# Kernel tuning notes

Hardware: AMD Instinct MI355X
Metric: run time of the kernel (lower is better)

Reference implementation:

```python
import jax, jax.numpy as jnp
import numpy as np

D_IN = 1024
D_OUT = 1024
N_HEADS = 16
D_K = D_OUT // N_HEADS
ROPE_THETA = 10000.0


def setup_inputs() -> dict:
    key = jax.random.key(0)
    ks = jax.random.split(key, 5)
    x = jax.random.normal(ks[0], (2, 2048, D_IN), dtype=jnp.float32)
    token_positions = jnp.arange(2048, dtype=jnp.int32)
    scale = 0.02
    wq = jax.random.normal(ks[1], (D_OUT, D_IN), dtype=jnp.float32) * scale
    wk = jax.random.normal(ks[2], (D_OUT, D_IN), dtype=jnp.float32) * scale
    wv = jax.random.normal(ks[3], (D_OUT, D_IN), dtype=jnp.float32) * scale
    wo = jax.random.normal(ks[4], (D_OUT, D_OUT), dtype=jnp.float32) * scale
    return {"x": x, "token_positions": token_positions, "wq": wq, "wk": wk, "wv": wv, "wo": wo}


def _rope(x, token_positions):
    # x: [..., S, d_k]; token_positions: [S]
    d_k = x.shape[-1]
    idx = jnp.arange(d_k)
    k = idx // 2
    # thetas[i, j] = pos_i / theta^(2*(j//2)/d_k)
    angles = token_positions[:, None].astype(x.dtype) / jnp.power(
        jnp.asarray(ROPE_THETA, x.dtype), 2.0 * k.astype(x.dtype) / d_k
    )  # [S, d_k]
    cos = jnp.cos(angles)
    sin = jnp.sin(angles) * jnp.where(idx % 2 == 0, -1.0, 1.0).astype(x.dtype)
    pair_swaps = idx + jnp.where(idx % 2 == 0, 1, -1)  # swap even/odd pairs
    return x * cos + x[..., pair_swaps] * sin


def _forward(x, token_positions, wq, wk, wv, wo):
    B, S, _ = x.shape
    # fused QKV projection (same math as concat + split)
    q = jnp.einsum("bsd,od->bso", x, wq)
    k = jnp.einsum("bsd,od->bso", x, wk)
    v = jnp.einsum("bsd,od->bso", x, wv)
    # split heads: [B, S, H*dk] -> [B, H, S, dk]
    split = lambda t: t.reshape(B, S, N_HEADS, D_K).transpose(0, 2, 1, 3)
    q, k, v = split(q), split(k), split(v)
    q = _rope(q, token_positions)
    k = _rope(k, token_positions)
    scores = jnp.einsum("bhqd,bhkd->bhqk", q, k) / jnp.sqrt(jnp.asarray(D_K, x.dtype))
    causal = jnp.tril(jnp.ones((S, S), dtype=bool))
    scores = jnp.where(causal, scores, -jnp.inf)
    probs = jax.nn.softmax(scores, axis=-1)
    ctx = jnp.einsum("bhqk,bhkd->bhqd", probs, v)
    merged = ctx.transpose(0, 2, 1, 3).reshape(B, S, D_OUT)
    return jnp.einsum("bsm,om->bso", merged, wo)


def reference(x, token_positions, wq, wk, wv, wo):
    return _forward(x, token_positions, wq, wk, wv, wo)
```

## Files before the change

### kernel.cpp

```cpp
#include <hip/hip_runtime.h>

#define D_MODEL 1024
#define SEQ     2048
#define BATCH   2
#define NHEADS  16
#define DK      64
#define NROWS   (BATCH*SEQ)

typedef unsigned short u16;
typedef __bf16 bf16x8 __attribute__((ext_vector_type(8)));
typedef float  f32x4  __attribute__((ext_vector_type(4)));

__device__ __forceinline__ u16 f2bf(float f) {
    union { float f; unsigned u; } v; v.f = f;
    unsigned u = v.u;
    u += 0x7fffu + ((u >> 16) & 1);
    return (u16)(u >> 16);
}
__device__ __forceinline__ float bf2f(u16 h) {
    union { unsigned u; float f; } v; v.u = ((unsigned)h) << 16;
    return v.f;
}
__device__ __forceinline__ unsigned cvtpk_bf16(float lo, float hi) {
    unsigned r;
    asm("v_cvt_pk_bf16_f32 %0, %1, %2" : "=v"(r) : "v"(lo), "v"(hi));
    return r;
}

__device__ __forceinline__ void gload_lds16(const u16* g, u16* l) {
    __builtin_amdgcn_global_load_lds(
        (const __attribute__((address_space(1))) void*)g,
        (__attribute__((address_space(3))) void*)l, 16, 0, 0);
}

__global__ void cvt_bf16_all(const float* __restrict__ x,
                             const float* __restrict__ w0, const float* __restrict__ w1,
                             const float* __restrict__ w2, const float* __restrict__ w3,
                             u16* __restrict__ xb, u16* __restrict__ wb) {
    int i = blockIdx.x * blockDim.x + threadIdx.x;
    int row = i >> 8;
    int c   = (i & 255) * 4;
    const float* src; u16* dst;
    if (row < 4096) {
        src = x + (size_t)row * 1024;
        dst = xb + (size_t)row * 1024;
    } else {
        int r2 = row - 4096;
        int ws = r2 >> 10;
        int rr = r2 & 1023;
        const float* wsrc = ws == 0 ? w0 : ws == 1 ? w1 : ws == 2 ? w2 : w3;
        src = wsrc + (size_t)rr * 1024;
        dst = wb + ((size_t)ws << 20) + (size_t)rr * 1024;
    }
    float4 v = *(const float4*)(src + c);
    uint2 o;
    o.x = (unsigned)f2bf(v.x) | ((unsigned)f2bf(v.y) << 16);
    o.y = (unsigned)f2bf(v.z) | ((unsigned)f2bf(v.w) << 16);
    *(uint2*)(dst + c) = o;
}

__global__ __launch_bounds__(256) void gemm_qkv_p(
    const u16* __restrict__ A, const u16* __restrict__ W,
    u16* __restrict__ Qp, u16* __restrict__ Kp, u16* __restrict__ Vt)
{
    __shared__ __align__(16) u16 Ash[128 * 32];
    __shared__ __align__(16) u16 Bsh[128 * 32];

    const int m0  = blockIdx.x * 128;
    const int sel = blockIdx.y >> 3;
    const int n0  = (blockIdx.y & 7) * 128;
    const u16* B = W + ((size_t)sel << 20);
    const int tid = threadIdx.x;
    const int lane = tid & 63;
    const int w    = tid >> 6;
    const int wr = w >> 1, wc = w & 1;
    const int fr = lane & 15;
    const int fk = (lane >> 4) * 8;
    const int rsub = lane >> 2;
    const int csub = (lane & 3) * 8;

    f32x4 acc[4][4];
#pragma unroll
    for (int i = 0; i < 4; ++i)
#pragma unroll
        for (int j = 0; j < 4; ++j) acc[i][j] = (f32x4){0.f, 0.f, 0.f, 0.f};

    for (int k0 = 0; k0 < 1024; k0 += 32) {
        __syncthreads();
        const u16* Ab = A + (size_t)(m0 + 16 * w + rsub) * 1024 + k0 + csub;
        const u16* Bb = B + (size_t)(n0 + 16 * w + rsub) * 1024 + k0 + csub;
#pragma unroll
        for (int half = 0; half < 2; ++half) {
            size_t ro = (size_t)(half * 64) * 1024;
            int lo = (half * 64 + 16 * w) * 32;
            gload_lds16(Ab + ro, &Ash[lo]);
            gload_lds16(Bb + ro, &Bsh[lo]);
        }
        __syncthreads();

        bf16x8 ah[4], bh[4];
#pragma unroll
        for (int i = 0; i < 4; ++i)
            ah[i] = *(const bf16x8*)&Ash[(wr * 64 + i * 16 + fr) * 32 + fk];
#pragma unroll
        for (int j = 0; j < 4; ++j)
            bh[j] = *(const bf16x8*)&Bsh[(wc * 64 + j * 16 + fr) * 32 + fk];
#pragma unroll
        for (int i = 0; i < 4; ++i)
#pragma unroll
            for (int j = 0; j < 4; ++j)
                acc[i][j] = __builtin_amdgcn_mfma_f32_16x16x32_bf16(ah[i], bh[j], acc[i][j], 0, 0, 0);
    }

    const int r0 = (lane >> 4) * 4;
#pragma unroll
    for (int i = 0; i < 4; ++i) {
#pragma unroll
        for (int j = 0; j < 4; ++j) {
            int col = n0 + wc * 64 + j * 16 + fr;
#pragma unroll
            for (int r = 0; r < 4; ++r) {
                int row = m0 + wr * 64 + i * 16 + r0 + r;
                u16 v = f2bf(acc[i][j][r]);
                if (sel == 0)      Qp[(size_t)row * 1024 + col] = v;
                else if (sel == 1) Kp[(size_t)row * 1024 + col] = v;
                else               Vt[(size_t)col * NROWS + row] = v;
            }
        }
    }
}

__global__ __launch_bounds__(256) void gemm_out_p(
    const u16* __restrict__ A, const u16* __restrict__ B, float* __restrict__ Cout)
{
    __shared__ __align__(16) u16 Ash[128 * 32];
    __shared__ __align__(16) u16 Bsh[128 * 32];

    const int m0 = blockIdx.x * 128;
    const int n0 = blockIdx.y * 128;
    const int tid = threadIdx.x;
    const int lane = tid & 63;
    const int w    = tid >> 6;
    const int wr = w >> 1, wc = w & 1;
    const int fr = lane & 15;
    const int fk = (lane >> 4) * 8;
    const int rsub = lane >> 2;
    const int csub = (lane & 3) * 8;

    f32x4 acc[4][4];
#pragma unroll
    for (int i = 0; i < 4; ++i)
#pragma unroll
        for (int j = 0; j < 4; ++j) acc[i][j] = (f32x4){0.f, 0.f, 0.f, 0.f};

    for (int k0 = 0; k0 < 1024; k0 += 32) {
        __syncthreads();
        const u16* Ab = A + (size_t)(m0 + 16 * w + rsub) * 1024 + k0 + csub;
        const u16* Bb = B + (size_t)(n0 + 16 * w + rsub) * 1024 + k0 + csub;
#pragma unroll
        for (int half = 0; half < 2; ++half) {
            size_t ro = (size_t)(half * 64) * 1024;
            int lo = (half * 64 + 16 * w) * 32;
            gload_lds16(Ab + ro, &Ash[lo]);
            gload_lds16(Bb + ro, &Bsh[lo]);
        }
        __syncthreads();

        bf16x8 ah[4], bh[4];
#pragma unroll
        for (int i = 0; i < 4; ++i)
            ah[i] = *(const bf16x8*)&Ash[(wr * 64 + i * 16 + fr) * 32 + fk];
#pragma unroll
        for (int j = 0; j < 4; ++j)
            bh[j] = *(const bf16x8*)&Bsh[(wc * 64 + j * 16 + fr) * 32 + fk];
#pragma unroll
        for (int i = 0; i < 4; ++i)
#pragma unroll
            for (int j = 0; j < 4; ++j)
                acc[i][j] = __builtin_amdgcn_mfma_f32_16x16x32_bf16(ah[i], bh[j], acc[i][j], 0, 0, 0);
    }

    const int r0 = (lane >> 4) * 4;
#pragma unroll
    for (int i = 0; i < 4; ++i) {
#pragma unroll
        for (int j = 0; j < 4; ++j) {
            int col = n0 + wc * 64 + j * 16 + fr;
#pragma unroll
            for (int r = 0; r < 4; ++r)
                Cout[(size_t)(m0 + wr * 64 + i * 16 + r0 + r) * 1024 + col] = acc[i][j][r];
        }
    }
}

__global__ void rope_plain(u16* __restrict__ qk, const int* __restrict__ pos) {
    int i = blockIdx.x * blockDim.x + threadIdx.x;
    int p = i & 511;
    int n = i >> 9;
    int s = n & 2047;
    int k = p & 31;
    int h = p >> 5;
    size_t base = (size_t)n * 1024 + h * DK + 2 * k;
    unsigned v = *(const unsigned*)&qk[base];
    float x0 = bf2f((u16)(v & 0xffff));
    float x1 = bf2f((u16)(v >> 16));
    float ang = (float)pos[s] * expf((float)k * -0.28782313662425575f);
    float c = cosf(ang), sn = sinf(ang);
    float qs = (n < 4096) ? 0.18033688011112042f : 1.0f;
    c *= qs; sn *= qs;
    float y0 = x0 * c - x1 * sn;
    float y1 = x1 * c + x0 * sn;
    *(unsigned*)&qk[base] = (unsigned)f2bf(y0) | ((unsigned)f2bf(y1) << 16);
}

__global__ __launch_bounds__(512, 4) void attn_v8(
    const u16* __restrict__ Qp, const u16* __restrict__ Kp, const u16* __restrict__ Vt,
    u16* __restrict__ Op, float* __restrict__ mlbuf)
{
    const int slot = 39 - (int)blockIdx.x;
    const int h = blockIdx.y, b = blockIdx.z;
    int g, rr;
    if (slot < 4)       { g = 0; rr = slot; }
    else if (slot < 12) { g = 1; rr = slot - 4; }
    else if (slot < 24) { g = 2; rr = slot - 12; }
    else                { g = 3; rr = slot - 24; }
    const int qq  = rr / (g + 1);
    const int qt2 = 4 * g + qq;
    const int c   = rr - qq * (g + 1);

    const int tid  = threadIdx.x;
    const int lane = tid & 63;
    const int w    = tid >> 6;
    const int fr = lane & 15;
    const int fg = lane >> 4;
    const int bS = b * SEQ;
    const int hd = h * DK;
    const int qbase = qt2 * 128 + 16 * w;
    const int ntk = 2 * qt2 + 2;
    const int kt0 = 8 * c;
    const int kt1 = min(8 * c + 8, ntk);

    __shared__ __align__(16) u16 Kl[2][64 * 64];
    __shared__ __align__(16) u16 Vl[2][64 * 64];
    __shared__ __align__(16) u16 Plds[8][16][72];

    const int dsrow  = 8 * w + (lane >> 3);
    const int lincol = (lane & 7) * 8;
    const int dsoff  = dsrow * 64 + (((lane & 7) ^ (lane >> 3)) * 8);
    const int swz    = (fr & 7) * 8;

    const u16* qrow = Qp + (size_t)(bS + qbase + fr) * 1024 + hd;
    bf16x8 qf0 = *(const bf16x8*)(qrow + fg * 8);
    bf16x8 qf1 = *(const bf16x8*)(qrow + 32 + fg * 8);

    f32x4 o[4];
#pragma unroll
    for (int j = 0; j < 4; ++j) o[j] = (f32x4){0.f, 0.f, 0.f, 0.f};
    float mrow = -1e30f, lrow = 0.f;

    uint4 kreg, vreg;
#define LOADR(KT) do { \
    kreg = *(const uint4*)(Kp + (size_t)(bS + (KT) * 64 + dsrow) * 1024 + hd + lincol); \
    vreg = *(const uint4*)(Vt + (size_t)(hd + dsrow) * NROWS + bS + (KT) * 64 + lincol); \
} while (0)
#define DSW(BUF) do { \
    *(uint4*)&Kl[BUF][dsoff] = kreg; \
    *(uint4*)&Vl[BUF][dsoff] = vreg; \
} while (0)

    LOADR(kt0);
    DSW(0);
    if (kt0 + 1 < kt1) LOADR(kt0 + 1);
    __syncthreads();

    int cur = 0;
    for (int kt = kt0; kt < kt1; ++kt) {
        if (kt + 1 < kt1) {
            DSW(cur ^ 1);
            if (kt + 2 < kt1) LOADR(kt + 2);
        }
        const int k0 = kt * 64;
        if (k0 <= qbase + 15) {
            bf16x8 kf[4][2];
#pragma unroll
            for (int t = 0; t < 4; ++t) {
                const u16* kr = &Kl[cur][(16 * t + fr) * 64];
                kf[t][0] = *(const bf16x8*)(kr + ((fg * 8) ^ swz));
                kf[t][1] = *(const bf16x8*)(kr + (((4 + fg) * 8) ^ swz));
            }
            f32x4 sc4[4];
            __builtin_amdgcn_s_setprio(1);
#pragma unroll
            for (int t = 0; t < 4; ++t) {
                f32x4 a = (f32x4){0.f, 0.f, 0.f, 0.f};
                a = __builtin_amdgcn_mfma_f32_16x16x32_bf16(kf[t][0], qf0, a, 0, 0, 0);
                a = __builtin_amdgcn_mfma_f32_16x16x32_bf16(kf[t][1], qf1, a, 0, 0, 0);
                sc4[t] = a;
            }
            __builtin_amdgcn_s_setprio(0);
            float p[4][4];
#pragma unroll
            for (int t = 0; t < 4; ++t)
#pragma unroll
                for (int r = 0; r < 4; ++r) p[t][r] = sc4[t][r];
            if (k0 + 63 > qbase) {
#pragma unroll
                for (int t = 0; t < 4; ++t)
#pragma unroll
                    for (int r = 0; r < 4; ++r)
                        if (k0 + 16 * t + 4 * fg + r > qbase + fr) p[t][r] = -1e30f;
            }
            float a0 = fmaxf(fmaxf(p[0][0], p[0][1]), fmaxf(p[0][2], p[0][3]));
            float a1 = fmaxf(fmaxf(p[1][0], p[1][1]), fmaxf(p[1][2], p[1][3]));
            float a2 = fmaxf(fmaxf(p[2][0], p[2][1]), fmaxf(p[2][2], p[2][3]));
            float a3 = fmaxf(fmaxf(p[3][0], p[3][1]), fmaxf(p[3][2], p[3][3]));
            float mx = fmaxf(fmaxf(a0, a1), fmaxf(a2, a3));
            mx = fmaxf(mx, __shfl_xor(mx, 16));
            mx = fmaxf(mx, __shfl_xor(mx, 32));
            float scf = 1.0f;
            if (!__all(mx <= mrow + 8.0f)) {
                float mnew = fmaxf(mrow, mx);
                scf = exp2f(mrow - mnew);
                float s0 = __shfl(scf, 4 * fg);
                float s1 = __shfl(scf, 4 * fg + 1);
                float s2 = __shfl(scf, 4 * fg + 2);
                float s3 = __shfl(scf, 4 * fg + 3);
#pragma unroll
                for (int j = 0; j < 4; ++j) {
                    o[j][0] *= s0; o[j][1] *= s1; o[j][2] *= s2; o[j][3] *= s3;
                }
                mrow = mnew;
            }
            float rs = 0.f;
#pragma unroll
            for (int t = 0; t < 4; ++t)
#pragma unroll
                for (int r = 0; r < 4; ++r) {
                    p[t][r] = exp2f(p[t][r] - mrow);
                    rs += p[t][r];
                }
            rs += __shfl_xor(rs, 16);
            rs += __shfl_xor(rs, 32);
            lrow = lrow * scf + rs;
#pragma unroll
            for (int t = 0; t < 4; ++t) {
                uint2 pk;
                pk.x = cvtpk_bf16(p[t][0], p[t][1]);
                pk.y = cvtpk_bf16(p[t][2], p[t][3]);
                *(uint2*)&Plds[w][fr][16 * t + 4 * fg] = pk;
            }
            bf16x8 pf0 = *(const bf16x8*)&Plds[w][fr][fg * 8];
            bf16x8 pf1 = *(const bf16x8*)&Plds[w][fr][32 + fg * 8];
            __builtin_amdgcn_s_setprio(1);
#pragma unroll
            for (int j = 0; j < 4; ++j) {
                const u16* vr = &Vl[cur][(16 * j + fr) * 64];
                bf16x8 v0 = *(const bf16x8*)(vr + ((fg * 8) ^ swz));
                bf16x8 v1 = *(const bf16x8*)(vr + (((4 + fg) * 8) ^ swz));
                o[j] = __builtin_amdgcn_mfma_f32_16x16x32_bf16(pf0, v0, o[j], 0, 0, 0);
                o[j] = __builtin_amdgcn_mfma_f32_16x16x32_bf16(pf1, v1, o[j], 0, 0, 0);
            }
            __builtin_amdgcn_s_setprio(0);
        }
        __syncthreads();
        cur ^= 1;
    }
#undef LOADR
#undef DSW

    const int slotg = (b * NHEADS + h) * 40 + slot;
#pragma unroll
    for (int r = 0; r < 4; ++r) {
        int rrel = 16 * w + 4 * fg + r;
#pragma unroll
        for (int j = 0; j < 4; ++j)
            Op[((size_t)slotg * 128 + rrel) * 64 + 16 * j + fr] = f2bf(o[j][r]);
    }
    if (fg == 0) {
        float* pp = mlbuf + ((size_t)slotg * 128 + 16 * w + fr) * 2;
        pp[0] = mrow;
        pp[1] = lrow;
    }
}

__global__ void attn_combine3(const u16* __restrict__ Op, const float* __restrict__ mlbuf,
                              u16* __restrict__ Mb) {
    int i = blockIdx.x * blockDim.x + threadIdx.x;
    int row = i >> 7;
    int c8  = (i & 127) * 8;
    int h   = c8 >> 6;
    int s   = row & 2047;
    int b   = row >> 11;
    int qt2 = s >> 7;
    int g   = qt2 >> 2;
    int nch = g + 1;
    int slot0 = (b * NHEADS + h) * 40 + 2 * g * (g + 1) + (qt2 & 3) * (g + 1);
    int rrel = s & 127, crel = c8 & 63;

    float mv[4], lv[4];
    float m = -1e30f;
    for (int k = 0; k < nch; ++k) {
        const float* pp = mlbuf + ((size_t)(slot0 + k) * 128 + rrel) * 2;
        mv[k] = pp[0]; lv[k] = pp[1];
        m = fmaxf(m, mv[k]);
    }
    float L = 0.f;
    for (int k = 0; k < nch; ++k) {
        mv[k] = exp2f(mv[k] - m);
        L += lv[k] * mv[k];
    }
    float acc[8];
#pragma unroll
    for (int jj = 0; jj < 8; ++jj) acc[jj] = 0.f;
    for (int k = 0; k < nch; ++k) {
        float wgt = mv[k];
        uint4 u = *(const uint4*)(Op + ((size_t)(slot0 + k) * 128 + rrel) * 64 + crel);
        const unsigned* wrd = (const unsigned*)&u;
#pragma unroll
        for (int kk = 0; kk < 4; ++kk) {
            acc[2 * kk]     += wgt * bf2f((u16)(wrd[kk] & 0xffff));
            acc[2 * kk + 1] += wgt * bf2f((u16)(wrd[kk] >> 16));
        }
    }
    float inv = 1.0f / L;
    unsigned ou[4];
#pragma unroll
    for (int kk = 0; kk < 4; ++kk)
        ou[kk] = (unsigned)f2bf(acc[2 * kk] * inv) | ((unsigned)f2bf(acc[2 * kk + 1] * inv) << 16);
    *(uint4*)(Mb + (size_t)row * 1024 + c8) = *(uint4*)ou;
}

extern "C" void kernel_launch(void* const* d_in, const int* in_sizes, int n_in,
                              void* d_out, int out_size, void* d_ws, size_t ws_size,
                              hipStream_t stream) {
    const float* x   = (const float*)d_in[0];
    const int*   pos = (const int*)d_in[1];
    const float* wq  = (const float*)d_in[2];
    const float* wk  = (const float*)d_in[3];
    const float* wv  = (const float*)d_in[4];
    const float* wo  = (const float*)d_in[5];
    float* out = (float*)d_out;

    char* ws = (char*)d_ws;
    u16* xb  = (u16*)(ws);
    u16* wb  = (u16*)(ws + (24ull << 20));
    u16* wob = wb + 3 * (1 << 20);
    u16* Qp  = (u16*)(ws + (32ull << 20));
    u16* Kp  = (u16*)(ws + (40ull << 20));
    u16* Vt  = (u16*)(ws + (48ull << 20));
    u16* Mb  = (u16*)(ws + (56ull << 20));
    u16* Op  = (u16*)(ws);
    float* mlbuf = (float*)(ws + (21ull << 20));

    cvt_bf16_all<<<8192, 256, 0, stream>>>(x, wq, wk, wv, wo, xb, wb);

    gemm_qkv_p<<<dim3(NROWS / 128, 24), 256, 0, stream>>>(xb, wb, Qp, Kp, Vt);

    rope_plain<<<16384, 256, 0, stream>>>(Qp, pos);

    attn_v8<<<dim3(40, NHEADS, BATCH), 512, 0, stream>>>(Qp, Kp, Vt, Op, mlbuf);
    attn_combine3<<<2048, 256, 0, stream>>>(Op, mlbuf, Mb);

    gemm_out_p<<<dim3(NROWS / 128, 8), 256, 0, stream>>>(Mb, wob, out);
}
```

Measured before the change: 153.5 us.

## Widen GEMM K-tile to 64 with XOR-swizzled LDS and staged V transpose

New measurement: 144.6 us. -5.8%, faster.

```diff
diff --git a/kernel.cpp b/kernel.cpp
--- a/kernel.cpp
+++ b/kernel.cpp
@@ -63,8 +63,9 @@
     const u16* __restrict__ A, const u16* __restrict__ W,
     u16* __restrict__ Qp, u16* __restrict__ Kp, u16* __restrict__ Vt)
 {
-    __shared__ __align__(16) u16 Ash[128 * 32];
-    __shared__ __align__(16) u16 Bsh[128 * 32];
+    __shared__ __align__(16) u16 SMEM[2 * 128 * 64];
+    u16* Ash = SMEM;
+    u16* Bsh = SMEM + 128 * 64;
 
     const int m0  = blockIdx.x * 128;
     const int sel = blockIdx.y >> 3;
@@ -75,9 +76,9 @@
     const int w    = tid >> 6;
     const int wr = w >> 1, wc = w & 1;
     const int fr = lane & 15;
-    const int fk = (lane >> 4) * 8;
-    const int rsub = lane >> 2;
-    const int csub = (lane & 3) * 8;
+    const int fg = lane >> 4;
+    const int strow = lane >> 3;
+    const int scol  = ((lane & 7) ^ strow) * 8;
 
     f32x4 acc[4][4];
 #pragma unroll
@@ -85,46 +86,74 @@
 #pragma unroll
         for (int j = 0; j < 4; ++j) acc[i][j] = (f32x4){0.f, 0.f, 0.f, 0.f};
 
-    for (int k0 = 0; k0 < 1024; k0 += 32) {
-        __syncthreads();
-        const u16* Ab = A + (size_t)(m0 + 16 * w + rsub) * 1024 + k0 + csub;
-        const u16* Bb = B + (size_t)(n0 + 16 * w + rsub) * 1024 + k0 + csub;
-#pragma unroll
-        for (int half = 0; half < 2; ++half) {
-            size_t ro = (size_t)(half * 64) * 1024;
-            int lo = (half * 64 + 16 * w) * 32;
-            gload_lds16(Ab + ro, &Ash[lo]);
-            gload_lds16(Bb + ro, &Bsh[lo]);
-        }
-        __syncthreads();
-
-        bf16x8 ah[4], bh[4];
+    for (int k0 = 0; k0 < 1024; k0 += 64) {
+        __syncthreads();
+#pragma unroll
+        for (int s = 0; s < 4; ++s) {
+            int st  = 4 * w + s;
+            int row = 8 * st + strow;
+            gload_lds16(A + (size_t)(m0 + row) * 1024 + k0 + scol, &Ash[8 * st * 64]);
+            gload_lds16(B + (size_t)(n0 + row) * 1024 + k0 + scol, &Bsh[8 * st * 64]);
+        }
+        __syncthreads();
+#pragma unroll
+        for (int kk = 0; kk < 2; ++kk) {
+            bf16x8 ah[4], bh[4];
+#pragma unroll
+            for (int i = 0; i < 4; ++i) {
+                int row = wr * 64 + i * 16 + fr;
+                ah[i] = *(const bf16x8*)&Ash[row * 64 + (((kk * 4 + fg) ^ (fr & 7)) * 8)];
+            }
+#pragma unroll
+            for (int j = 0; j < 4; ++j) {
+                int row = wc * 64 + j * 16 + fr;
+                bh[j] = *(const bf16x8*)&Bsh[row * 64 + (((kk * 4 + fg) ^ (fr & 7)) * 8)];
+            }
+#pragma unroll
+            for (int i = 0; i < 4; ++i)
+#pragma unroll
+                for (int j = 0; j < 4; ++j)
+                    acc[i][j] = __builtin_amdgcn_mfma_f32_16x16x32_bf16(ah[i], bh[j], acc[i][j], 0, 0, 0);
+        }
+    }
+
+    const int r0 = fg * 4;
+    if (sel == 2) {
+        __syncthreads();
+        u16* CT = SMEM;
 #pragma unroll
         for (int i = 0; i < 4; ++i)
-            ah[i] = *(const bf16x8*)&Ash[(wr * 64 + i * 16 + fr) * 32 + fk];
-#pragma unroll
-        for (int j = 0; j < 4; ++j)
-            bh[j] = *(const bf16x8*)&Bsh[(wc * 64 + j * 16 + fr) * 32 + fk];
-#pragma unroll
-        for (int i = 0; i < 4; ++i)
-#pragma unroll
-            for (int j = 0; j < 4; ++j)
-                acc[i][j] = __builtin_amdgcn_mfma_f32_16x16x32_bf16(ah[i], bh[j], acc[i][j], 0, 0, 0);
-    }
-
-    const int r0 = (lane >> 4) * 4;
-#pragma unroll
-    for (int i = 0; i < 4; ++i) {
-#pragma unroll
-        for (int j = 0; j < 4; ++j) {
-            int col = n0 + wc * 64 + j * 16 + fr;
-#pragma unroll
-            for (int r = 0; r < 4; ++r) {
-                int row = m0 + wr * 64 + i * 16 + r0 + r;
-                u16 v = f2bf(acc[i][j][r]);
-                if (sel == 0)      Qp[(size_t)row * 1024 + col] = v;
-                else if (sel == 1) Kp[(size_t)row * 1024 + col] = v;
-                else               Vt[(size_t)col * NROWS + row] = v;
+#pragma unroll
+            for (int j = 0; j < 4; ++j) {
+                int colr = wc * 64 + j * 16 + fr;
+#pragma unroll
+                for (int r = 0; r < 4; ++r) {
+                    int rowr = wr * 64 + i * 16 + r0 + r;
+                    int ch = (rowr >> 3) ^ (colr & 15);
+                    CT[colr * 128 + ch * 8 + (rowr & 7)] = f2bf(acc[i][j][r]);
+                }
+            }
+        __syncthreads();
+        const int colr = tid >> 1;
+        const int half = tid & 1;
+        u16* dst = Vt + (size_t)(n0 + colr) * NROWS + m0 + half * 64;
+#pragma unroll
+        for (int cc = 0; cc < 8; ++cc) {
+            int ch = (half * 8 + cc) ^ (colr & 15);
+            *(uint4*)(dst + cc * 8) = *(const uint4*)&CT[colr * 128 + ch * 8];
+        }
+    } else {
+        u16* Outp = (sel == 0) ? Qp : Kp;
+#pragma unroll
+        for (int i = 0; i < 4; ++i) {
+#pragma unroll
+            for (int j = 0; j < 4; ++j) {
+                int col = n0 + wc * 64 + j * 16 + fr;
+#pragma unroll
+                for (int r = 0; r < 4; ++r) {
+                    int row = m0 + wr * 64 + i * 16 + r0 + r;
+                    Outp[(size_t)row * 1024 + col] = f2bf(acc[i][j][r]);
+                }
             }
         }
     }
@@ -133,8 +162,9 @@
 __global__ __launch_bounds__(256) void gemm_out_p(
     const u16* __restrict__ A, const u16* __restrict__ B, float* __restrict__ Cout)
 {
-    __shared__ __align__(16) u16 Ash[128 * 32];
-    __shared__ __align__(16) u16 Bsh[128 * 32];
+    __shared__ __align__(16) u16 SMEM[2 * 128 * 64];
+    u16* Ash = SMEM;
+    u16* Bsh = SMEM + 128 * 64;
 
     const int m0 = blockIdx.x * 128;
     const int n0 = blockIdx.y * 128;
@@ -143,9 +173,9 @@
     const int w    = tid >> 6;
     const int wr = w >> 1, wc = w & 1;
     const int fr = lane & 15;
-    const int fk = (lane >> 4) * 8;
-    const int rsub = lane >> 2;
-    const int csub = (lane & 3) * 8;
+    const int fg = lane >> 4;
+    const int strow = lane >> 3;
+    const int scol  = ((lane & 7) ^ strow) * 8;
 
     f32x4 acc[4][4];
 #pragma unroll
@@ -153,34 +183,38 @@
 #pragma unroll
         for (int j = 0; j < 4; ++j) acc[i][j] = (f32x4){0.f, 0.f, 0.f, 0.f};
 
-    for (int k0 = 0; k0 < 1024; k0 += 32) {
-        __syncthreads();
-        const u16* Ab = A + (size_t)(m0 + 16 * w + rsub) * 1024 + k0 + csub;
-        const u16* Bb = B + (size_t)(n0 + 16 * w + rsub) * 1024 + k0 + csub;
-#pragma unroll
-        for (int half = 0; half < 2; ++half) {
-            size_t ro = (size_t)(half * 64) * 1024;
-            int lo = (half * 64 + 16 * w) * 32;
-            gload_lds16(Ab + ro, &Ash[lo]);
-            gload_lds16(Bb + ro, &Bsh[lo]);
-        }
-        __syncthreads();
-
-        bf16x8 ah[4], bh[4];
-#pragma unroll
-        for (int i = 0; i < 4; ++i)
-            ah[i] = *(const bf16x8*)&Ash[(wr * 64 + i * 16 + fr) * 32 + fk];
-#pragma unroll
-        for (int j = 0; j < 4; ++j)
-            bh[j] = *(const bf16x8*)&Bsh[(wc * 64 + j * 16 + fr) * 32 + fk];
-#pragma unroll
-        for (int i = 0; i < 4; ++i)
-#pragma unroll
-            for (int j = 0; j < 4; ++j)
-                acc[i][j] = __builtin_amdgcn_mfma_f32_16x16x32_bf16(ah[i], bh[j], acc[i][j], 0, 0, 0);
-    }
-
-    const int r0 = (lane >> 4) * 4;
+    for (int k0 = 0; k0 < 1024; k0 += 64) {
+        __syncthreads();
+#pragma unroll
+        for (int s = 0; s < 4; ++s) {
+            int st  = 4 * w + s;
+            int row = 8 * st + strow;
+            gload_lds16(A + (size_t)(m0 + row) * 1024 + k0 + scol, &Ash[8 * st * 64]);
+            gload_lds16(B + (size_t)(n0 + row) * 1024 + k0 + scol, &Bsh[8 * st * 64]);
+        }
+        __syncthreads();
+#pragma unroll
+        for (int kk = 0; kk < 2; ++kk) {
+            bf16x8 ah[4], bh[4];
+#pragma unroll
+            for (int i = 0; i < 4; ++i) {
+                int row = wr * 64 + i * 16 + fr;
+                ah[i] = *(const bf16x8*)&Ash[row * 64 + (((kk * 4 + fg) ^ (fr & 7)) * 8)];
+            }
+#pragma unroll
+            for (int j = 0; j < 4; ++j) {
+                int row = wc * 64 + j * 16 + fr;
+                bh[j] = *(const bf16x8*)&Bsh[row * 64 + (((kk * 4 + fg) ^ (fr & 7)) * 8)];
+            }
+#pragma unroll
+            for (int i = 0; i < 4; ++i)
+#pragma unroll
+                for (int j = 0; j < 4; ++j)
+                    acc[i][j] = __builtin_amdgcn_mfma_f32_16x16x32_bf16(ah[i], bh[j], acc[i][j], 0, 0, 0);
+        }
+    }
+
+    const int r0 = fg * 4;
 #pragma unroll
     for (int i = 0; i < 4; ++i) {
 #pragma unroll
```
